# Optimization experiments

Measured on AMD Instinct MI355X. Metric: run time of the kernel, lower is better.

The kernel has to match this reference:

```python
import jax, jax.numpy as jnp
import numpy as np

K = 1024        # n_embeddings
D = 256         # embedding_dim
BETA = 0.25
EPS = 1e-10


def setup_inputs() -> dict:
    key = jax.random.key(0)
    k1, k2 = jax.random.split(key)
    inputs = jax.random.normal(k1, (64, D, 32, 32), dtype=jnp.float32)
    # codebook init matches nn.Embedding.weight.data.uniform_(-1/K, 1/K)
    embedding = jax.random.uniform(k2, (K, D), dtype=jnp.float32,
                                   minval=-1.0 / K, maxval=1.0 / K)
    return {"inputs": inputs, "embedding": embedding}


def reference(inputs, embedding):
    B, C, H, W = inputs.shape  # C == D
    # NCHW -> NHWC -> (N, D)
    z = jnp.transpose(inputs, (0, 2, 3, 1)).reshape(-1, C)
    N = z.shape[0]

    # squared distances ||z - e||^2 = ||z||^2 + ||e||^2 - 2 z.e  (GEMM-dominant)
    d = (jnp.sum(z * z, axis=1, keepdims=True)
         + jnp.sum(embedding * embedding, axis=1)[None, :]
         - 2.0 * (z @ embedding.T))                     # (N, K)
    idx = jnp.argmin(d, axis=1)                          # (N,) int

    z_q = embedding[idx]                                 # gather (N, D)

    # codebook + commitment loss
    loss = (jnp.mean((jax.lax.stop_gradient(z_q) - z) ** 2)
            + BETA * jnp.mean((z_q - jax.lax.stop_gradient(z)) ** 2))

    # straight-through estimator
    z_q_st = z + jax.lax.stop_gradient(z_q - z)

    # perplexity over codebook usage
    counts = jnp.zeros((K,), dtype=z.dtype).at[idx].add(1.0)
    probs = counts / N
    perplexity = jnp.exp(-jnp.sum(probs * jnp.log(probs + EPS)))

    z_q_out = jnp.transpose(z_q_st.reshape(B, H, W, C), (0, 3, 1, 2))
    return loss, z_q_out, perplexity
```

## Files before the change

kernel.cpp:

```cpp
#include <hip/hip_runtime.h>

#define D_   256
#define HW_  1024
#define N_   65536
#define K_   1024
#define ND_  16777216
#define MARGIN_A 2.0e-6f
#define MARGIN_B 3.5e-5f

typedef __attribute__((ext_vector_type(8))) short bf16x8;
typedef __attribute__((ext_vector_type(8))) _Float16 f16x8;
typedef __attribute__((ext_vector_type(4))) float f32x4;

union f16cv { _Float16 h; unsigned short u; };

__device__ inline unsigned short f16_bits(float v) {
    f16cv c; c.h = (_Float16)v; return c.u;
}

#define GLL16(g, l) __builtin_amdgcn_global_load_lds( \
    (const __attribute__((address_space(1))) unsigned int*)(const void*)(g), \
    (__attribute__((address_space(3))) unsigned int*)(void*)(l), 16, 0, 0)

__global__ __launch_bounds__(256) void k_startup(const float* __restrict__ Z,
                                                 const float* __restrict__ E,
                                                 unsigned short* __restrict__ Eh,
                                                 float* __restrict__ Et,
                                                 float* __restrict__ e2f,
                                                 double* __restrict__ e2d,
                                                 unsigned short* __restrict__ Zh,
                                                 float* __restrict__ S1,
                                                 double* __restrict__ zpart,
                                                 int* __restrict__ counts,
                                                 int* __restrict__ nflag_f,
                                                 int* __restrict__ nflag_c,
                                                 double* __restrict__ loss_acc) {
    int t = threadIdx.x;
    if (blockIdx.x < 1024) {
        __shared__ double sh[256];
        int k = blockIdx.x;
        float v = E[(size_t)k * D_ + t];
        Eh[(size_t)k * D_ + t] = f16_bits(v * 1024.f);
        Et[(size_t)t * K_ + k] = v;
        sh[t] = (double)v * v;
        __syncthreads();
        for (int off = 128; off; off >>= 1) {
            if (t < off) sh[t] += sh[t + off];
            __syncthreads();
        }
        if (t == 0) { e2f[k] = (float)sh[0]; e2d[k] = sh[0]; }
        if (k < 4) counts[k * 256 + t] = 0;
        else if (k == 4 && t == 0) { *nflag_f = 0; *nflag_c = 0; *loss_acc = 0.0; }
        return;
    }
    __shared__ unsigned short lh[32][264];
    __shared__ float sabs[32][32];
    __shared__ double dsh[256];
    int bid = blockIdx.x - 1024;
    int b = bid >> 5, hw0 = (bid & 31) * 32;
    int qd = t & 7, ds = t >> 3;
    const float* zb = Z + (size_t)b * (D_ * HW_) + hw0 + 4 * qd;
    float a0 = 0.f, a1 = 0.f, a2 = 0.f, a3 = 0.f;
    double qsum = 0.0;
    #pragma unroll
    for (int j = 0; j < 8; ++j) {
        int d = ds + 32 * j;
        float4 v = *(const float4*)(zb + (size_t)d * HW_);
        lh[4 * qd + 0][d] = f16_bits(v.x);
        lh[4 * qd + 1][d] = f16_bits(v.y);
        lh[4 * qd + 2][d] = f16_bits(v.z);
        lh[4 * qd + 3][d] = f16_bits(v.w);
        a0 += fabsf(v.x); a1 += fabsf(v.y); a2 += fabsf(v.z); a3 += fabsf(v.w);
        qsum = fma((double)v.x, (double)v.x, qsum);
        qsum = fma((double)v.y, (double)v.y, qsum);
        qsum = fma((double)v.z, (double)v.z, qsum);
        qsum = fma((double)v.w, (double)v.w, qsum);
    }
    sabs[4 * qd + 0][ds] = a0;
    sabs[4 * qd + 1][ds] = a1;
    sabs[4 * qd + 2][ds] = a2;
    sabs[4 * qd + 3][ds] = a3;
    dsh[t] = qsum;
    __syncthreads();
    for (int off = 128; off; off >>= 1) {
        if (t < off) dsh[t] += dsh[t + off];
        __syncthreads();
    }
    if (t == 0) zpart[bid] = dsh[0];

    int row = t >> 3, cb = t & 7;
    size_t nbase = ((size_t)b * HW_ + hw0 + row) * D_;
    #pragma unroll
    for (int jj = 0; jj < 4; ++jj) {
        int ch = cb + jj * 8;
        *(bf16x8*)(Zh + nbase + ch * 8) = *(const bf16x8*)&lh[row][ch * 8];
    }
    if (t < 32) {
        float s = 0.f;
        #pragma unroll
        for (int q = 0; q < 32; ++q) s += sabs[t][q];
        S1[(size_t)b * HW_ + hw0 + t] = s;
    }
}

__global__ __launch_bounds__(256) void k_phase1(const unsigned short* __restrict__ Zh,
                                                const unsigned short* __restrict__ Eh,
                                                const float* __restrict__ e2f,
                                                float* __restrict__ pm1,
                                                float* __restrict__ pm2,
                                                int* __restrict__ pi1) {
    __shared__ __align__(16) unsigned short lds[4 * 8192];
    int t = threadIdx.x, w = t >> 6, l = t & 63;
    int bid = blockIdx.x;
    int xcd = bid & 7, slot = bid >> 3;
    int mb = xcd * 64 + (slot >> 3);
    int nb = slot & 7;
    int wr = w >> 1, wc = w & 1;

    const unsigned short* src =
        (w < 2 ? Zh + (size_t)mb * 128 * D_ : Eh + (size_t)nb * 128 * D_)
        + (size_t)(w & 1) * 64 * D_;
    unsigned short* myl0 = &lds[__builtin_amdgcn_readfirstlane(w * 4096)];
    unsigned short* myl1 = &lds[__builtin_amdgcn_readfirstlane(16384 + w * 4096)];

    int Rl = l >> 3;
    int lc = (l & 7) ^ (l >> 3);

    f32x4 acc[4][4];
    #pragma unroll
    for (int m = 0; m < 4; ++m)
        #pragma unroll
        for (int nn = 0; nn < 4; ++nn) acc[m][nn] = (f32x4){0.f, 0.f, 0.f, 0.f};

    for (int ktp = 0; ktp < 2; ++ktp) {
        #pragma unroll
        for (int i = 0; i < 8; ++i) {
            const unsigned short* g = src + (size_t)(i * 8 + Rl) * D_ + (ktp * 2) * 64 + lc * 8;
            GLL16(g, myl0 + i * 512);
        }
        #pragma unroll
        for (int i = 0; i < 8; ++i) {
            const unsigned short* g = src + (size_t)(i * 8 + Rl) * D_ + (ktp * 2 + 1) * 64 + lc * 8;
            GLL16(g, myl1 + i * 512);
        }
        __syncthreads();
        int q = l >> 4;
        #pragma unroll
        for (int kt2 = 0; kt2 < 2; ++kt2) {
            const char* Ab = (const char*)lds + kt2 * 32768;
            const char* Bb = Ab + 16384;
            #pragma unroll
            for (int ks2 = 0; ks2 < 2; ++ks2) {
                int pcb = ((ks2 * 4 + q) ^ (l & 7)) * 16;
                f16x8 ah[4];
                #pragma unroll
                for (int m = 0; m < 4; ++m)
                    ah[m] = *(const f16x8*)(Ab + (wr * 64 + m * 16 + (l & 15)) * 128 + pcb);
                #pragma unroll
                for (int nn = 0; nn < 4; ++nn) {
                    f16x8 bh = *(const f16x8*)(Bb + (wc * 64 + nn * 16 + (l & 15)) * 128 + pcb);
                    #pragma unroll
                    for (int m = 0; m < 4; ++m)
                        acc[m][nn] = __builtin_amdgcn_mfma_f32_16x16x32_f16(ah[m], bh, acc[m][nn], 0, 0, 0);
                }
            }
        }
        __syncthreads();
    }

    float m1v[4][4], m2v[4][4]; int i1v[4][4];
    #pragma unroll
    for (int m = 0; m < 4; ++m)
        #pragma unroll
        for (int r = 0; r < 4; ++r) { m1v[m][r] = 3.4e38f; m2v[m][r] = 3.4e38f; i1v[m][r] = 0; }

    #pragma unroll
    for (int nn = 0; nn < 4; ++nn) {
        int c = nb * 128 + wc * 64 + nn * 16 + (l & 15);
        float e2 = e2f[c];
        #pragma unroll
        for (int m = 0; m < 4; ++m)
            #pragma unroll
            for (int r = 0; r < 4; ++r) {
                float s = fmaf(-2.f / 1024.f, acc[m][nn][r], e2);
                if (s < m1v[m][r])      { m2v[m][r] = m1v[m][r]; m1v[m][r] = s; i1v[m][r] = c; }
                else if (s < m2v[m][r]) { m2v[m][r] = s; }
            }
    }
    #pragma unroll
    for (int off = 1; off < 16; off <<= 1) {
        #pragma unroll
        for (int m = 0; m < 4; ++m)
            #pragma unroll
            for (int r = 0; r < 4; ++r) {
                float o1 = __shfl_xor(m1v[m][r], off, 64);
                float o2 = __shfl_xor(m2v[m][r], off, 64);
                int   oi = __shfl_xor(i1v[m][r], off, 64);
                if (o1 < m1v[m][r]) { m2v[m][r] = fminf(m1v[m][r], o2); m1v[m][r] = o1; i1v[m][r] = oi; }
                else                { m2v[m][r] = fminf(m2v[m][r], o1); }
            }
    }
    __syncthreads();
    float* ex1 = (float*)lds;
    float* ex2 = ex1 + 256;
    int*   exi = (int*)(ex2 + 256);
    if ((l & 15) == 0) {
        int qq = l >> 4;
        #pragma unroll
        for (int m = 0; m < 4; ++m)
            #pragma unroll
            for (int r = 0; r < 4; ++r) {
                int e = (wr * 2 + wc) * 64 + m * 16 + qq * 4 + r;
                ex1[e] = m1v[m][r]; ex2[e] = m2v[m][r]; exi[e] = i1v[m][r];
            }
    }
    __syncthreads();
    if (t < 128) {
        int wr2 = t >> 6, rw = t & 63;
        int e0 = (wr2 * 2 + 0) * 64 + rw, e1 = (wr2 * 2 + 1) * 64 + rw;
        float a1 = ex1[e0], a2 = ex2[e0]; int ai = exi[e0];
        float b1 = ex1[e1], b2 = ex2[e1]; int bi = exi[e1];
        float M1, M2; int I1;
        if (a1 <= b1) { M1 = a1; I1 = ai; M2 = fminf(a2, b1); }
        else          { M1 = b1; I1 = bi; M2 = fminf(b2, a1); }
        size_t p = (size_t)nb * N_ + (size_t)mb * 128 + t;
        pm1[p] = M1; pm2[p] = M2; pi1[p] = I1;
    }
}

__global__ __launch_bounds__(256) void k_merge(const float* __restrict__ pm1,
                                               const float* __restrict__ pm2,
                                               const int* __restrict__ pi1,
                                               const float* __restrict__ S1,
                                               const double* __restrict__ zpart,
                                               int* __restrict__ idx,
                                               int* __restrict__ counts,
                                               int* __restrict__ c8,
                                               unsigned char* __restrict__ ncand,
                                               int* __restrict__ list_c,
                                               int* __restrict__ nflag_c,
                                               int* __restrict__ list_f,
                                               int* __restrict__ nflag_f,
                                               double* __restrict__ loss_acc) {
    __shared__ double msh[256];
    int n = blockIdx.x * 256 + threadIdx.x;
    float a1[8], a2[8]; int ai[8];
    float M1 = 3.4e38f, M2 = 3.4e38f; int I1 = 0;
    #pragma unroll
    for (int nb = 0; nb < 8; ++nb) {
        size_t p = (size_t)nb * N_ + n;
        a1[nb] = pm1[p]; a2[nb] = pm2[p]; ai[nb] = pi1[p];
        if (a1[nb] < M1) { M2 = fminf(M1, a2[nb]); M1 = a1[nb]; I1 = ai[nb]; }
        else             { M2 = fminf(M2, a1[nb]); }
    }
    idx[n] = I1;
    atomicAdd(&counts[I1], 1);
    float thr = M1 + fmaf(S1[n], MARGIN_A, MARGIN_B);
    bool fl = M2 < thr;
    bool needfull = false;
    int cnt = 0;
    if (fl) {
        #pragma unroll
        for (int nb = 0; nb < 8; ++nb) {
            if (a2[nb] < thr) needfull = true;
            if (a1[nb] < thr) ++cnt;
        }
    }
    bool candrow = fl && !needfull;
    bool fullrow = fl && needfull;
    if (candrow) {
        ncand[n] = (unsigned char)cnt;
        int pos = 0;
        #pragma unroll
        for (int nb = 0; nb < 8; ++nb)
            if (a1[nb] < thr) c8[(size_t)n * 8 + (pos++)] = ai[nb];
    }
    int lane = threadIdx.x & 63;
    unsigned long long mc = __ballot(candrow);
    if (mc) {
        int base = 0;
        if (lane == 0) base = atomicAdd(nflag_c, __popcll(mc));
        base = __shfl(base, 0, 64);
        if (candrow) list_c[base + __popcll(mc & ((1ull << lane) - 1ull))] = n;
    }
    unsigned long long mf = __ballot(fullrow);
    if (mf) {
        int base = 0;
        if (lane == 0) base = atomicAdd(nflag_f, __popcll(mf));
        base = __shfl(base, 0, 64);
        if (fullrow) list_f[base + __popcll(mf & ((1ull << lane) - 1ull))] = n;
    }
    double m1loss = (double)M1;
    if (blockIdx.x == 0) {
        double zs = 0.0;
        #pragma unroll
        for (int j = 0; j < 8; ++j) zs += zpart[threadIdx.x + 256 * j];
        m1loss += zs;
    }
    msh[threadIdx.x] = m1loss;
    __syncthreads();
    for (int off = 128; off; off >>= 1) {
        if (threadIdx.x < off) msh[threadIdx.x] += msh[threadIdx.x + off];
        __syncthreads();
    }
    if (threadIdx.x == 0) atomicAdd(loss_acc, msh[0]);
}

__global__ __launch_bounds__(256) void k_fixup(const float* __restrict__ Z,
                                               const float* __restrict__ E,
                                               const float* __restrict__ Et,
                                               const double* __restrict__ e2d,
                                               const int* __restrict__ c8,
                                               const unsigned char* __restrict__ ncand,
                                               const int* __restrict__ list_c,
                                               const int* __restrict__ nflag_c,
                                               const int* __restrict__ list_f,
                                               const int* __restrict__ nflag_f,
                                               int* __restrict__ idx,
                                               int* __restrict__ counts) {
    __shared__ float  zs[8][257];
    __shared__ int    sn[8];
    __shared__ double rbv[8][4];
    __shared__ int    rbi[8][4];
    int t = threadIdx.x, w = t >> 6, l = t & 63;

    if (blockIdx.x >= 1024) {
        int nf = *nflag_c;
        int gw = (blockIdx.x - 1024) * 4 + w;
        for (int ii = gw; ii < nf; ii += 1024) {
            int n = list_c[ii];
            int b = n >> 10, hw = n & (HW_ - 1);
            const float* zp = Z + (size_t)b * (D_ * HW_) + hw;
            double z0 = (double)zp[(size_t)(l      ) * HW_];
            double z1 = (double)zp[(size_t)(l +  64) * HW_];
            double z2 = (double)zp[(size_t)(l + 128) * HW_];
            double z3 = (double)zp[(size_t)(l + 192) * HW_];
            int nc = ncand[n];
            double bv = 1e300; int bi = 0;
            for (int j = 0; j < nc; ++j) {
                int c = c8[(size_t)n * 8 + j];
                const float* er = E + (size_t)c * D_;
                double s = z0 * (double)er[l];
                s = fma(z1, (double)er[l +  64], s);
                s = fma(z2, (double)er[l + 128], s);
                s = fma(z3, (double)er[l + 192], s);
                #pragma unroll
                for (int off = 32; off; off >>= 1) s += __shfl_xor(s, off, 64);
                double sc = fma(-2.0, s, e2d[c]);
                if (sc < bv || (sc == bv && c < bi)) { bv = sc; bi = c; }
            }
            if (l == 0) {
                int old = idx[n];
                if (bi != old) {
                    idx[n] = bi;
                    atomicSub(&counts[old], 1);
                    atomicAdd(&counts[bi], 1);
                }
            }
        }
        return;
    }

    int nf = *nflag_f;
    double ed0 = e2d[4 * t + 0], ed1 = e2d[4 * t + 1];
    double ed2 = e2d[4 * t + 2], ed3 = e2d[4 * t + 3];

    for (int ch = blockIdx.x; ch * 8 < nf; ch += 1024) {
        __syncthreads();
        int i0 = ch * 8;
        int vc = min(8, nf - i0);
        if (t < 8) sn[t] = list_f[i0 + min(t, vc - 1)];
        __syncthreads();

        #pragma unroll
        for (int j = 0; j < 8; ++j) {
            int n = sn[j];
            zs[j][t] = Z[(size_t)(n >> 10) * (D_ * HW_) + (size_t)t * HW_ + (n & (HW_ - 1))];
        }
        __syncthreads();

        double s[8][4];
        #pragma unroll
        for (int r = 0; r < 8; ++r)
            s[r][0] = s[r][1] = s[r][2] = s[r][3] = 0.0;

        for (int d0 = 0; d0 < 256; d0 += 8) {
            float4 e4v[8];
            #pragma unroll
            for (int u = 0; u < 8; ++u)
                e4v[u] = *(const float4*)(Et + (size_t)(d0 + u) * K_ + 4 * t);
            #pragma unroll
            for (int u = 0; u < 8; ++u) {
                double ex = (double)e4v[u].x, ey = (double)e4v[u].y;
                double ez = (double)e4v[u].z, ew = (double)e4v[u].w;
                #pragma unroll
                for (int r = 0; r < 8; ++r) {
                    double zv = (double)zs[r][d0 + u];
                    s[r][0] = fma(zv, ex, s[r][0]);
                    s[r][1] = fma(zv, ey, s[r][1]);
                    s[r][2] = fma(zv, ez, s[r][2]);
                    s[r][3] = fma(zv, ew, s[r][3]);
                }
            }
        }

        #pragma unroll
        for (int r = 0; r < 8; ++r) {
            double bv = fma(-2.0, s[r][0], ed0); int bi = 4 * t;
            double c1 = fma(-2.0, s[r][1], ed1);
            double c2 = fma(-2.0, s[r][2], ed2);
            double c3 = fma(-2.0, s[r][3], ed3);
            if (c1 < bv) { bv = c1; bi = 4 * t + 1; }
            if (c2 < bv) { bv = c2; bi = 4 * t + 2; }
            if (c3 < bv) { bv = c3; bi = 4 * t + 3; }
            #pragma unroll
            for (int off = 1; off < 64; off <<= 1) {
                double ov = __shfl_xor(bv, off, 64);
                int    oi = __shfl_xor(bi, off, 64);
                if (ov < bv || (ov == bv && oi < bi)) { bv = ov; bi = oi; }
            }
            if (l == 0) { rbv[r][w] = bv; rbi[r][w] = bi; }
        }
        __syncthreads();

        if (t < vc) {
            double bv = rbv[t][0]; int bi = rbi[t][0];
            #pragma unroll
            for (int ww = 1; ww < 4; ++ww) {
                double ov = rbv[t][ww]; int oi = rbi[t][ww];
                if (ov < bv || (ov == bv && oi < bi)) { bv = ov; bi = oi; }
            }
            int n = sn[t];
            int old = idx[n];
            if (bi != old) {
                idx[n] = bi;
                atomicSub(&counts[old], 1);
                atomicAdd(&counts[bi], 1);
            }
        }
    }
}

__global__ __launch_bounds__(256) void k_gatherfinal(const float* __restrict__ E,
                                                     const int* __restrict__ idx,
                                                     const int* __restrict__ counts,
                                                     const double* __restrict__ loss_acc,
                                                     float* __restrict__ out) {
    int t = threadIdx.x;
    if (blockIdx.x == 2048) {
        __shared__ double sh[256];
        double s = 0.0;
        for (int k = t; k < K_; k += 256) {
            double p = (double)counts[k] / (double)N_;
            s += p * log(p + 1e-10);
        }
        sh[t] = s; __syncthreads();
        for (int off = 128; off; off >>= 1) {
            if (t < off) sh[t] += sh[t + off];
            __syncthreads();
        }
        if (t == 0) {
            out[0]       = (float)((*loss_acc) / (double)ND_ * 1.25);
            out[1 + ND_] = (float)exp(-sh[0]);
        }
        return;
    }
    __shared__ float ecache[32][257];
    __shared__ int sidx[32];
    int n0 = blockIdx.x * 32;
    int b = n0 >> 10, hw0 = n0 & (HW_ - 1);
    if (t < 32) sidx[t] = idx[n0 + t];
    __syncthreads();
    #pragma unroll 8
    for (int j = 0; j < 32; ++j)
        ecache[j][t] = E[(size_t)sidx[j] * D_ + t];
    __syncthreads();
    int hw = t & 31, cq = t >> 5;
    float* ob = out + 1 + (size_t)b * (D_ * HW_) + hw0 + hw;
    #pragma unroll 8
    for (int jj = 0; jj < 32; ++jj) {
        int c = cq * 32 + jj;
        ob[(size_t)c * HW_] = ecache[hw][c];
    }
}

extern "C" void kernel_launch(void* const* d_in, const int* in_sizes, int n_in,
                              void* d_out, int out_size, void* d_ws, size_t ws_size,
                              hipStream_t stream) {
    (void)in_sizes; (void)n_in; (void)out_size; (void)ws_size;
    const float* Z = (const float*)d_in[0];
    const float* E = (const float*)d_in[1];
    float* out = (float*)d_out;

    char* ws = (char*)d_ws;
    unsigned short* Zh       = (unsigned short*)(ws);
    unsigned short* Eh       = (unsigned short*)(ws + 33554432);
    float*          Et       = (float*)(ws + 34078720);
    float*          e2f      = (float*)(ws + 35127296);
    double*         e2d      = (double*)(ws + 35131392);
    float*          S1       = (float*)(ws + 35139584);
    float*          pm1      = (float*)(ws + 35401728);
    float*          pm2      = (float*)(ws + 37498880);
    int*            pi1      = (int*)  (ws + 39596032);
    int*            idx      = (int*)  (ws + 41693184);
    int*            list_f   = (int*)  (ws + 41955328);
    int*            list_c   = (int*)  (ws + 42217472);
    int*            c8       = (int*)  (ws + 42479616);
    unsigned char*  ncand    = (unsigned char*)(ws + 44576768);
    int*            counts   = (int*)  (ws + 44642304);
    int*            nflag_f  = (int*)  (ws + 44646400);
    int*            nflag_c  = (int*)  (ws + 44646464);
    double*         loss_acc = (double*)(ws + 44646528);
    double*         zpart    = (double*)(ws + 44646592);

    k_startup    <<<dim3(3072), dim3(256), 0, stream>>>(Z, E, Eh, Et, e2f, e2d, Zh, S1,
                                                        zpart, counts, nflag_f, nflag_c, loss_acc);
    k_phase1     <<<dim3(4096), dim3(256), 0, stream>>>(Zh, Eh, e2f, pm1, pm2, pi1);
    k_merge      <<<dim3(256),  dim3(256), 0, stream>>>(pm1, pm2, pi1, S1, zpart, idx, counts,
                                                        c8, ncand, list_c, nflag_c, list_f, nflag_f, loss_acc);
    k_fixup      <<<dim3(1280), dim3(256), 0, stream>>>(Z, E, Et, e2d, c8, ncand,
                                                        list_c, nflag_c, list_f, nflag_f, idx, counts);
    k_gatherfinal<<<dim3(2049), dim3(256), 0, stream>>>(E, idx, counts, loss_acc, out);
}
```

Measured before the change: 213.3 us.

## Fuse merge kernel into phase1 via last-block-done counter per row tile

Removes the separate k_merge launch. Each phase1 block writes its partial (min1, min2, index) as one packed float4, then bumps a per-row-tile atomic counter, and the last of the 8 column blocks performs the merge, candidate listing and loss accumulation. The zpart sum moves into the final kernel. This saves a kernel launch and the tail gap between launches, and lets merge work overlap with other GEMM blocks, at the cost of extra fences, atomics and serial merge work on the last-arriving blocks.

After: 511.3 us. 140% more time.

```diff
diff --git a/kernel.cpp b/kernel.cpp
--- a/kernel.cpp
+++ b/kernel.cpp
@@ -34,6 +34,7 @@
                                                  int* __restrict__ counts,
                                                  int* __restrict__ nflag_f,
                                                  int* __restrict__ nflag_c,
+                                                 int* __restrict__ done,
                                                  double* __restrict__ loss_acc) {
     int t = threadIdx.x;
     if (blockIdx.x < 1024) {
@@ -51,6 +52,7 @@
         if (t == 0) { e2f[k] = (float)sh[0]; e2d[k] = sh[0]; }
         if (k < 4) counts[k * 256 + t] = 0;
         else if (k == 4 && t == 0) { *nflag_f = 0; *nflag_c = 0; *loss_acc = 0.0; }
+        else if (k == 5) { done[t] = 0; done[256 + t] = 0; }
         return;
     }
     __shared__ unsigned short lh[32][264];
@@ -106,10 +108,20 @@
 __global__ __launch_bounds__(256) void k_phase1(const unsigned short* __restrict__ Zh,
                                                 const unsigned short* __restrict__ Eh,
                                                 const float* __restrict__ e2f,
-                                                float* __restrict__ pm1,
-                                                float* __restrict__ pm2,
-                                                int* __restrict__ pi1) {
+                                                const float* __restrict__ S1,
+                                                float4* __restrict__ pmq,
+                                                int* __restrict__ idx,
+                                                int* __restrict__ counts,
+                                                int* __restrict__ c8,
+                                                unsigned char* __restrict__ ncand,
+                                                int* __restrict__ list_c,
+                                                int* __restrict__ nflag_c,
+                                                int* __restrict__ list_f,
+                                                int* __restrict__ nflag_f,
+                                                int* __restrict__ done,
+                                                double* __restrict__ loss_acc) {
     __shared__ __align__(16) unsigned short lds[4 * 8192];
+    __shared__ int slast;
     int t = threadIdx.x, w = t >> 6, l = t & 63;
     int bid = blockIdx.x;
     int xcd = bid & 7, slot = bid >> 3;
@@ -224,86 +236,73 @@
         if (a1 <= b1) { M1 = a1; I1 = ai; M2 = fminf(a2, b1); }
         else          { M1 = b1; I1 = bi; M2 = fminf(b2, a1); }
         size_t p = (size_t)nb * N_ + (size_t)mb * 128 + t;
-        pm1[p] = M1; pm2[p] = M2; pi1[p] = I1;
-    }
-}
-
-__global__ __launch_bounds__(256) void k_merge(const float* __restrict__ pm1,
-                                               const float* __restrict__ pm2,
-                                               const int* __restrict__ pi1,
-                                               const float* __restrict__ S1,
-                                               const double* __restrict__ zpart,
-                                               int* __restrict__ idx,
-                                               int* __restrict__ counts,
-                                               int* __restrict__ c8,
-                                               unsigned char* __restrict__ ncand,
-                                               int* __restrict__ list_c,
-                                               int* __restrict__ nflag_c,
-                                               int* __restrict__ list_f,
-                                               int* __restrict__ nflag_f,
-                                               double* __restrict__ loss_acc) {
-    __shared__ double msh[256];
-    int n = blockIdx.x * 256 + threadIdx.x;
-    float a1[8], a2[8]; int ai[8];
-    float M1 = 3.4e38f, M2 = 3.4e38f; int I1 = 0;
-    #pragma unroll
-    for (int nb = 0; nb < 8; ++nb) {
-        size_t p = (size_t)nb * N_ + n;
-        a1[nb] = pm1[p]; a2[nb] = pm2[p]; ai[nb] = pi1[p];
-        if (a1[nb] < M1) { M2 = fminf(M1, a2[nb]); M1 = a1[nb]; I1 = ai[nb]; }
-        else             { M2 = fminf(M2, a1[nb]); }
-    }
-    idx[n] = I1;
-    atomicAdd(&counts[I1], 1);
-    float thr = M1 + fmaf(S1[n], MARGIN_A, MARGIN_B);
-    bool fl = M2 < thr;
-    bool needfull = false;
-    int cnt = 0;
-    if (fl) {
-        #pragma unroll
-        for (int nb = 0; nb < 8; ++nb) {
-            if (a2[nb] < thr) needfull = true;
-            if (a1[nb] < thr) ++cnt;
-        }
-    }
-    bool candrow = fl && !needfull;
-    bool fullrow = fl && needfull;
-    if (candrow) {
-        ncand[n] = (unsigned char)cnt;
-        int pos = 0;
-        #pragma unroll
-        for (int nb = 0; nb < 8; ++nb)
-            if (a1[nb] < thr) c8[(size_t)n * 8 + (pos++)] = ai[nb];
-    }
-    int lane = threadIdx.x & 63;
-    unsigned long long mc = __ballot(candrow);
-    if (mc) {
-        int base = 0;
-        if (lane == 0) base = atomicAdd(nflag_c, __popcll(mc));
-        base = __shfl(base, 0, 64);
-        if (candrow) list_c[base + __popcll(mc & ((1ull << lane) - 1ull))] = n;
-    }
-    unsigned long long mf = __ballot(fullrow);
-    if (mf) {
-        int base = 0;
-        if (lane == 0) base = atomicAdd(nflag_f, __popcll(mf));
-        base = __shfl(base, 0, 64);
-        if (fullrow) list_f[base + __popcll(mf & ((1ull << lane) - 1ull))] = n;
-    }
-    double m1loss = (double)M1;
-    if (blockIdx.x == 0) {
-        double zs = 0.0;
-        #pragma unroll
-        for (int j = 0; j < 8; ++j) zs += zpart[threadIdx.x + 256 * j];
-        m1loss += zs;
-    }
-    msh[threadIdx.x] = m1loss;
+        pmq[p] = make_float4(M1, M2, __int_as_float(I1), 0.f);
+    }
+
+    __threadfence();
+    if (t == 0) slast = atomicAdd(&done[mb], 1);
+    __syncthreads();
+    if (slast != 7) return;
+    __threadfence();
+
+    double m1loss = 0.0;
+    if (t < 128) {
+        int n = mb * 128 + t;
+        float a1v[8], a2v[8]; int aiv[8];
+        float M1 = 3.4e38f, M2 = 3.4e38f; int I1 = 0;
+        #pragma unroll
+        for (int q8 = 0; q8 < 8; ++q8) {
+            float4 v = pmq[(size_t)q8 * N_ + n];
+            a1v[q8] = v.x; a2v[q8] = v.y; aiv[q8] = __float_as_int(v.z);
+            if (v.x < M1) { M2 = fminf(M1, v.y); M1 = v.x; I1 = aiv[q8]; }
+            else          { M2 = fminf(M2, v.x); }
+        }
+        idx[n] = I1;
+        atomicAdd(&counts[I1], 1);
+        float thr = M1 + fmaf(S1[n], MARGIN_A, MARGIN_B);
+        bool fl = M2 < thr;
+        bool needfull = false;
+        int cnt = 0;
+        if (fl) {
+            #pragma unroll
+            for (int q8 = 0; q8 < 8; ++q8) {
+                if (a2v[q8] < thr) needfull = true;
+                if (a1v[q8] < thr) ++cnt;
+            }
+        }
+        bool candrow = fl && !needfull;
+        bool fullrow = fl && needfull;
+        if (candrow) {
+            ncand[n] = (unsigned char)cnt;
+            int pos = 0;
+            #pragma unroll
+            for (int q8 = 0; q8 < 8; ++q8)
+                if (a1v[q8] < thr) c8[(size_t)n * 8 + (pos++)] = aiv[q8];
+        }
+        unsigned long long mc = __ballot(candrow);
+        if (mc) {
+            int base = 0;
+            if (l == 0) base = atomicAdd(nflag_c, __popcll(mc));
+            base = __shfl(base, 0, 64);
+            if (candrow) list_c[base + __popcll(mc & ((1ull << l) - 1ull))] = n;
+        }
+        unsigned long long mf = __ballot(fullrow);
+        if (mf) {
+            int base = 0;
+            if (l == 0) base = atomicAdd(nflag_f, __popcll(mf));
+            base = __shfl(base, 0, 64);
+            if (fullrow) list_f[base + __popcll(mf & ((1ull << l) - 1ull))] = n;
+        }
+        m1loss = (double)M1;
+    }
+    double* msh = (double*)lds;
+    msh[t] = m1loss;
     __syncthreads();
     for (int off = 128; off; off >>= 1) {
-        if (threadIdx.x < off) msh[threadIdx.x] += msh[threadIdx.x + off];
-        __syncthreads();
-    }
-    if (threadIdx.x == 0) atomicAdd(loss_acc, msh[0]);
+        if (t < off) msh[t] += msh[t + off];
+        __syncthreads();
+    }
+    if (t == 0) atomicAdd(loss_acc, msh[0]);
 }
 
 __global__ __launch_bounds__(256) void k_fixup(const float* __restrict__ Z,
@@ -444,23 +443,28 @@
 __global__ __launch_bounds__(256) void k_gatherfinal(const float* __restrict__ E,
                                                      const int* __restrict__ idx,
                                                      const int* __restrict__ counts,
+                                                     const double* __restrict__ zpart,
                                                      const double* __restrict__ loss_acc,
                                                      float* __restrict__ out) {
     int t = threadIdx.x;
     if (blockIdx.x == 2048) {
-        __shared__ double sh[256];
+        __shared__ double sh[256], sh2[256];
         double s = 0.0;
         for (int k = t; k < K_; k += 256) {
             double p = (double)counts[k] / (double)N_;
             s += p * log(p + 1e-10);
         }
-        sh[t] = s; __syncthreads();
+        double zs = 0.0;
+        #pragma unroll
+        for (int j = 0; j < 8; ++j) zs += zpart[t + 256 * j];
+        sh[t] = s; sh2[t] = zs;
+        __syncthreads();
         for (int off = 128; off; off >>= 1) {
-            if (t < off) sh[t] += sh[t + off];
+            if (t < off) { sh[t] += sh[t + off]; sh2[t] += sh2[t + off]; }
             __syncthreads();
         }
         if (t == 0) {
-            out[0]       = (float)((*loss_acc) / (double)ND_ * 1.25);
+            out[0]       = (float)(((*loss_acc) + sh2[0]) / (double)ND_ * 1.25);
             out[1 + ND_] = (float)exp(-sh[0]);
         }
         return;
@@ -499,26 +503,25 @@
     float*          e2f      = (float*)(ws + 35127296);
     double*         e2d      = (double*)(ws + 35131392);
     float*          S1       = (float*)(ws + 35139584);
-    float*          pm1      = (float*)(ws + 35401728);
-    float*          pm2      = (float*)(ws + 37498880);
-    int*            pi1      = (int*)  (ws + 39596032);
-    int*            idx      = (int*)  (ws + 41693184);
-    int*            list_f   = (int*)  (ws + 41955328);
-    int*            list_c   = (int*)  (ws + 42217472);
-    int*            c8       = (int*)  (ws + 42479616);
-    unsigned char*  ncand    = (unsigned char*)(ws + 44576768);
-    int*            counts   = (int*)  (ws + 44642304);
-    int*            nflag_f  = (int*)  (ws + 44646400);
-    int*            nflag_c  = (int*)  (ws + 44646464);
-    double*         loss_acc = (double*)(ws + 44646528);
-    double*         zpart    = (double*)(ws + 44646592);
+    float4*         pmq      = (float4*)(ws + 35401728);
+    int*            idx      = (int*)  (ws + 43790336);
+    int*            list_f   = (int*)  (ws + 44052480);
+    int*            list_c   = (int*)  (ws + 44314624);
+    int*            c8       = (int*)  (ws + 44576768);
+    unsigned char*  ncand    = (unsigned char*)(ws + 46673920);
+    int*            counts   = (int*)  (ws + 46739456);
+    int*            nflag_f  = (int*)  (ws + 46743552);
+    int*            nflag_c  = (int*)  (ws + 46743616);
+    double*         loss_acc = (double*)(ws + 46743680);
+    double*         zpart    = (double*)(ws + 46743744);
+    int*            done     = (int*)  (ws + 46760128);
 
     k_startup    <<<dim3(3072), dim3(256), 0, stream>>>(Z, E, Eh, Et, e2f, e2d, Zh, S1,
-                                                        zpart, counts, nflag_f, nflag_c, loss_acc);
-    k_phase1     <<<dim3(4096), dim3(256), 0, stream>>>(Zh, Eh, e2f, pm1, pm2, pi1);
-    k_merge      <<<dim3(256),  dim3(256), 0, stream>>>(pm1, pm2, pi1, S1, zpart, idx, counts,
-                                                        c8, ncand, list_c, nflag_c, list_f, nflag_f, loss_acc);
+                                                        zpart, counts, nflag_f, nflag_c, done, loss_acc);
+    k_phase1     <<<dim3(4096), dim3(256), 0, stream>>>(Zh, Eh, e2f, S1, pmq, idx, counts,
+                                                        c8, ncand, list_c, nflag_c, list_f, nflag_f,
+                                                        done, loss_acc);
     k_fixup      <<<dim3(1280), dim3(256), 0, stream>>>(Z, E, Et, e2d, c8, ncand,
                                                         list_c, nflag_c, list_f, nflag_f, idx, counts);
-    k_gatherfinal<<<dim3(2049), dim3(256), 0, stream>>>(E, idx, counts, loss_acc, out);
+    k_gatherfinal<<<dim3(2049), dim3(256), 0, stream>>>(E, idx, counts, zpart, loss_acc, out);
 }
```
